# Optimization experiments

Hardware: AMD Instinct MI355X
Metric: run time of the kernel (lower is better)

## Reference

```python
import jax, jax.numpy as jnp
import numpy as np

CTX_LEN = 7
TAU = 2.0      # curr_temp = max_temp at init
ALPHA = -1.0   # dist_to_logits_alpha


def _prelu(v, a):
    return jnp.where(v >= 0, v, a * v)


def setup_inputs() -> dict:
    key = jax.random.key(0)
    ks = jax.random.split(key, 8)
    B, T, D, M = 8, 4096, 256, 1024
    x = jax.random.normal(ks[0], (B, T, D), dtype=jnp.float32)
    noise = jax.random.normal(ks[1], (B, D, T - 1 + CTX_LEN), dtype=jnp.float32)
    gumbel_u = jax.random.uniform(ks[2], (B * T, M), dtype=jnp.float32)
    embedding = jax.random.uniform(ks[3], (1, M, D), dtype=jnp.float32)  # nn.init.uniform_
    w_ctx = jax.random.normal(ks[4], (D, D, CTX_LEN), dtype=jnp.float32) * 0.02
    w_f1 = jax.random.normal(ks[5], (D, 2 * D), dtype=jnp.float32) * 0.04
    w_f2 = jax.random.normal(ks[6], (D, 2 * D), dtype=jnp.float32) * 0.04
    a1 = jnp.array(0.5, dtype=jnp.float32)
    a2 = jnp.array(0.5, dtype=jnp.float32)
    return {"x": x, "noise": noise, "gumbel_u": gumbel_u, "epo": 10,
            "embedding": embedding, "w_ctx": w_ctx, "w_f1": w_f1, "a1": a1,
            "w_f2": w_f2, "a2": a2}


def reference(x, noise, gumbel_u, epo, embedding, w_ctx, w_f1, a1, w_f2, a2):
    B, T, D = x.shape
    E = embedding[0]                      # [M, D]
    M = E.shape[0]
    xt = jnp.transpose(x, (0, 2, 1))      # [B, D, T]
    # context input: x[:, :-1] permuted, left-padded by 1+7-1=7, detached
    ctx_in = jax.lax.stop_gradient(jnp.pad(xt[:, :, :T - 1], ((0, 0), (0, 0), (CTX_LEN, 0))))
    scale = jnp.sqrt(jnp.mean(ctx_in ** 2, axis=(1, 2), keepdims=True))
    ctx_in_noisy = jax.lax.stop_gradient(ctx_in + 0.5 * scale * noise * (0.5 ** (epo / 10.0)))
    ctx_out = jax.lax.conv_general_dilated(
        ctx_in_noisy, w_ctx, (1,), 'VALID',
        dimension_numbers=('NCH', 'OIH', 'NCH'))   # [B, D, T]
    # fuse 1 (1x1 conv == channel matmul) + PReLU
    cat1 = jnp.concatenate([xt, ctx_out], axis=1)            # [B, 2D, T]
    cur = _prelu(jnp.einsum('oc,bct->bot', w_f1, cat1), a1)  # [B, D, T]
    cur = jnp.transpose(cur, (0, 2, 1)).reshape(-1, D)       # [B*T, D]
    # squared distances via addmm equivalent, scaled to logits
    dist = (jnp.sum(cur ** 2, axis=1, keepdims=True)
            + jnp.sum(E ** 2, axis=1)
            - 2.0 * cur @ E.T)                               # [B*T, M]
    dm = ALPHA * dist
    # hard code usage entropy
    k = jnp.argmax(dm, axis=-1)
    hard_probs = jnp.mean(jax.nn.one_hot(k, M, dtype=dm.dtype), axis=0)
    code_perplexity = -jnp.sum(hard_probs * jnp.log2(hard_probs + 1e-10))
    # soft usage entropy
    avg_probs = jnp.mean(jax.nn.softmax(dm, axis=-1), axis=0)
    prob_perplexity = -jnp.sum(avg_probs * jnp.log2(avg_probs + 1e-10))
    # hard gumbel-softmax (straight-through)
    u = jnp.clip(gumbel_u, 1e-10, 1.0 - 1e-7)
    g = -jnp.log(-jnp.log(u))
    y_soft = jax.nn.softmax((dm + g) / TAU, axis=-1)
    idx = jnp.argmax(y_soft, axis=-1)
    y_hard = jax.nn.one_hot(idx, M, dtype=y_soft.dtype)
    dm_st = y_hard - jax.lax.stop_gradient(y_soft) + y_soft  # [B*T, M]
    quantization_inds = idx.reshape(B, T, 1)
    # dequantize: one-hot (straight-through) times codebook
    out_q = (dm_st @ E).reshape(B, T, D)
    # fuse 2 + PReLU
    cat2 = jnp.concatenate([jnp.transpose(out_q, (0, 2, 1)), ctx_out], axis=1)
    quantized = jnp.transpose(_prelu(jnp.einsum('oc,bct->bot', w_f2, cat2), a2), (0, 2, 1))
    return quantized, code_perplexity, prob_perplexity, quantization_inds
```

## Files before the change

kernel.cpp:

```cpp
#include <hip/hip_runtime.h>
#include <cmath>

#define B_    8
#define T_    4096
#define D_    256
#define M_    1024
#define L_    4102
#define LP_   4104
#define CTX_  7
#define NROW_ 32768

constexpr size_t OFF_DM    = 0;
constexpr size_t OFF_XT    = 0;
constexpr size_t OFF_CTXN  = 33554432;
constexpr size_t OFF_CURT  = 33554432;
constexpr size_t OFF_CTXO  = OFF_CTXN + (size_t)B_ * D_ * LP_;
constexpr size_t OFF_CUR2  = OFF_CTXO + (size_t)B_ * D_ * T_;
constexpr size_t OFF_SOFT  = OFF_CUR2 + NROW_;
constexpr size_t OFF_HIST  = OFF_SOFT + 4096;
constexpr size_t OFF_SUMSQ = OFF_HIST + 1024;
constexpr size_t OFF_ESQ   = OFF_SUMSQ + 16;
constexpr size_t OFF_IDX   = OFF_ESQ + 1024;
constexpr size_t OFF_ET    = OFF_IDX + NROW_;
constexpr size_t OFF_W1T   = OFF_ET + 262144;
constexpr size_t OFF_W2T   = OFF_W1T + 131072;
constexpr size_t OFF_WCT   = OFF_W2T + 131072;
constexpr size_t OFF_P     = OFF_WCT + 458752;

using s16x8 = __attribute__((ext_vector_type(8))) short;
using f32x4 = __attribute__((ext_vector_type(4))) float;

__device__ __forceinline__ ushort bf16rne(float f) {
  uint u = __float_as_uint(f);
  u += 0x7fffu + ((u >> 16) & 1u);
  return (ushort)(u >> 16);
}
__device__ __forceinline__ float bf16tof(ushort h) {
  return __uint_as_float((uint)h << 16);
}

__global__ __launch_bounds__(256) void k_prep(const float* __restrict__ emb,
                                              const float* __restrict__ wf1,
                                              const float* __restrict__ wf2,
                                              const float* __restrict__ wctx,
                                              const float* __restrict__ x,
                                              float* __restrict__ ET,
                                              float* __restrict__ W1T,
                                              float* __restrict__ W2T,
                                              ushort* __restrict__ WPF,
                                              float* __restrict__ esq,
                                              float* __restrict__ sumsq) {
  const int id = blockIdx.x;
  if (id < 512) {
    __shared__ float tile[32][33];
    const int tx = threadIdx.x & 31, ty = threadIdx.x >> 5;
    const float* src; float* dst; int R, C, c0, r0;
    if (id < 256)      { src = emb;  dst = ET;  R = 1024; C = 256;  c0 = (id & 7) << 5;  r0 = (id >> 3) << 5; }
    else if (id < 384) { const int r = id - 256; src = wf1; dst = W1T; R = 256; C = 512; c0 = (r & 15) << 5; r0 = (r >> 4) << 5; }
    else               { const int r = id - 384; src = wf2; dst = W2T; R = 256; C = 512; c0 = (r & 15) << 5; r0 = (r >> 4) << 5; }
    for (int rr = ty; rr < 32; rr += 8) {
      const int rI = r0 + rr, cI = c0 + tx;
      tile[rr][tx] = (rI < R && cI < C) ? src[(size_t)rI * C + cI] : 0.f;
    }
    __syncthreads();
    for (int rr = ty; rr < 32; rr += 8) {
      const int cI = c0 + rr, rI = r0 + tx;
      if (cI < C && rI < R) dst[(size_t)cI * R + rI] = tile[tx][rr];
    }
  } else if (id < 736) {
    const int K8 = id - 512;
    const int h = K8 >> 5, j = K8 & 31;
    const int o = threadIdx.x;
    uint hp[4], lp[4];
    #pragma unroll
    for (int e2 = 0; e2 < 4; ++e2) {
      ushort hs[2], ls[2];
      #pragma unroll
      for (int k = 0; k < 2; ++k) {
        const int i = (j << 3) + (e2 << 1) + k;
        const float v = wctx[(size_t)o * 1792 + (size_t)i * 7 + h];
        const ushort hb = bf16rne(v);
        hs[k] = hb;
        ls[k] = bf16rne(v - bf16tof(hb));
      }
      hp[e2] = (uint)hs[0] | ((uint)hs[1] << 16);
      lp[e2] = (uint)ls[0] | ((uint)ls[1] << 16);
    }
    uint4* W = (uint4*)WPF;
    W[(size_t)(K8 * 2) * 256 + o]     = make_uint4(hp[0], hp[1], hp[2], hp[3]);
    W[(size_t)(K8 * 2 + 1) * 256 + o] = make_uint4(lp[0], lp[1], lp[2], lp[3]);
  } else if (id < 992) {
    const int row = ((id - 736) << 2) + (threadIdx.x >> 6);
    const int lane = threadIdx.x & 63;
    const float4 v = ((const float4*)emb)[((size_t)row << 6) + lane];
    float s = v.x * v.x + v.y * v.y + v.z * v.z + v.w * v.w;
    #pragma unroll
    for (int off = 32; off; off >>= 1) s += __shfl_down(s, off, 64);
    if (lane == 0) esq[row] = s;
  } else {
    const int chunk = id - 992;
    const int b = chunk >> 6, sub = chunk & 63;
    const float4* xb = (const float4*)(x + (size_t)b * T_ * D_);
    const int N4 = (T_ - 1) * D_ / 4;
    float s = 0.f;
    for (int j = sub * 256 + threadIdx.x; j < N4; j += 64 * 256) {
      float4 v = xb[j];
      s += v.x * v.x + v.y * v.y + v.z * v.z + v.w * v.w;
    }
    #pragma unroll
    for (int off = 32; off; off >>= 1) s += __shfl_down(s, off, 64);
    __shared__ float red[4];
    const int lane = threadIdx.x & 63, wv = threadIdx.x >> 6;
    if (lane == 0) red[wv] = s;
    __syncthreads();
    if (threadIdx.x == 0) atomicAdd(&sumsq[b], (red[0] + red[1]) + (red[2] + red[3]));
  }
}

__global__ __launch_bounds__(256) void k_noisy(const float* __restrict__ x,
                                               const float* __restrict__ noise,
                                               const int* __restrict__ epo,
                                               const float* __restrict__ sumsq,
                                               ushort* __restrict__ inT,
                                               float* __restrict__ xT) {
  const int b = blockIdx.z;
  const int i0 = blockIdx.y << 5;
  const int tau0 = blockIdx.x << 5;
  const int tx = threadIdx.x & 31, ty = threadIdx.x >> 5;
  __shared__ float xt[32][33];
  __shared__ float nz[32][33];
  const int tr0 = tau0 - CTX_;
  for (int r = ty; r < 32; r += 8) {
    const int t = tr0 + r;
    xt[r][tx] = (t >= 0 && t < T_) ? x[((size_t)b * T_ + t) * D_ + i0 + tx] : 0.f;
  }
  for (int r = ty; r < 32; r += 8) {
    const int tau = tau0 + tx;
    nz[r][tx] = (tau < L_) ? noise[((size_t)b * D_ + i0 + r) * L_ + tau] : 0.f;
  }
  __syncthreads();
  const float scale = sqrtf(sumsq[b] * (1.0f / (256.0f * 4102.0f)));
  const float coef = 0.5f * powf(0.5f, (float)epo[0] * 0.1f) * scale;
  for (int r = ty; r < 32; r += 8) {
    const int i = i0 + r;
    const int tau = tau0 + tx;
    const float xv = xt[tx][r];
    if (tau >= CTX_ && tau < T_ + CTX_)
      xT[((size_t)b * D_ + i) * T_ + (tau - CTX_)] = xv;
  }
  if (threadIdx.x < 128) {
    const int tau_r = threadIdx.x >> 2, jl = threadIdx.x & 3;
    const int tau = tau0 + tau_r;
    if (tau < L_) {
      uint hp[4], lp[4];
      #pragma unroll
      for (int e2 = 0; e2 < 4; ++e2) {
        ushort hs[2], ls[2];
        #pragma unroll
        for (int k = 0; k < 2; ++k) {
          const int ir = (jl << 3) + (e2 << 1) + k;
          const float v = coef * nz[ir][tau_r] + xt[tau_r][ir];
          const ushort hb = bf16rne(v);
          hs[k] = hb;
          ls[k] = bf16rne(v - bf16tof(hb));
        }
        hp[e2] = (uint)hs[0] | ((uint)hs[1] << 16);
        lp[e2] = (uint)ls[0] | ((uint)ls[1] << 16);
      }
      const int j = (i0 >> 3) + jl;
      const int jsw = j ^ (tau & 7);
      ushort* dst = inT + ((size_t)b * LP_ + tau) * 256 + (jsw << 3);
      *(uint4*)dst = make_uint4(hp[0], hp[1], hp[2], hp[3]);
      *(uint4*)(dst + (size_t)B_ * LP_ * 256) = make_uint4(lp[0], lp[1], lp[2], lp[3]);
    }
  }
}

__global__ __launch_bounds__(256, 2) void k_convm(const ushort* __restrict__ WPF,
                                                  const ushort* __restrict__ inT,
                                                  float* __restrict__ ctxo) {
  const int t0 = blockIdx.x << 6;
  const int b  = blockIdx.y;
  const int tid = threadIdx.x;
  const int lane = tid & 63;
  const int wv = tid >> 6;
  const int ln = lane & 15, lg = lane >> 4;
  __shared__ ushort sB[2 * 72 * 256];
  {
    const size_t rb = ((size_t)b * LP_ + t0) * 256;
    const uint4* s4h = (const uint4*)(inT + rb);
    const uint4* s4l = (const uint4*)(inT + (size_t)B_ * LP_ * 256 + rb);
    uint4* d4 = (uint4*)sB;
    for (int q = tid; q < 2304; q += 256) d4[q] = s4h[q];
    for (int q = tid; q < 2304; q += 256) d4[2304 + q] = s4l[q];
  }
  __syncthreads();

  const f32x4 fz = {0.f, 0.f, 0.f, 0.f};
  f32x4 acc[4][4];
  #pragma unroll
  for (int i = 0; i < 4; ++i)
    #pragma unroll
    for (int j = 0; j < 4; ++j) acc[i][j] = fz;

  const ushort* wp = WPF + ((size_t)lg * 512 + (wv << 6) + ln) * 8;

  #pragma unroll 1
  for (int h = 0; h < 7; ++h) {
    #pragma unroll 1
    for (int js = 0; js < 8; ++js) {
      const int K8b = (h << 5) + (js << 2);
      s16x8 Af[2][4];
      #pragma unroll
      for (int to = 0; to < 4; ++to) {
        const ushort* ap = wp + (size_t)(K8b * 512 + (to << 4)) * 8;
        Af[0][to] = *(const s16x8*)ap;
        Af[1][to] = *(const s16x8*)(ap + 2048);
      }
      s16x8 Bf[2][4];
      #pragma unroll
      for (int tt = 0; tt < 4; ++tt) {
        const int r = (tt << 4) + ln + h;
        const int jsw = ((js << 2) + lg) ^ (r & 7);
        const int e0 = r * 256 + (jsw << 3);
        Bf[0][tt] = *(const s16x8*)&sB[e0];
        Bf[1][tt] = *(const s16x8*)&sB[18432 + e0];
      }
      #pragma unroll
      for (int to = 0; to < 4; ++to)
        #pragma unroll
        for (int tt = 0; tt < 4; ++tt) {
          acc[to][tt] = __builtin_amdgcn_mfma_f32_16x16x32_bf16(Af[0][to], Bf[0][tt], acc[to][tt], 0, 0, 0);
          acc[to][tt] = __builtin_amdgcn_mfma_f32_16x16x32_bf16(Af[0][to], Bf[1][tt], acc[to][tt], 0, 0, 0);
          acc[to][tt] = __builtin_amdgcn_mfma_f32_16x16x32_bf16(Af[1][to], Bf[0][tt], acc[to][tt], 0, 0, 0);
        }
    }
  }
  float* cb = ctxo + ((size_t)b * 256 + (wv << 6)) * T_ + t0;
  #pragma unroll
  for (int to = 0; to < 4; ++to)
    #pragma unroll
    for (int tt = 0; tt < 4; ++tt)
      #pragma unroll
      for (int rg = 0; rg < 4; ++rg) {
        const int o_loc = (to << 4) + (lg << 2) + rg;
        cb[(size_t)o_loc * T_ + (tt << 4) + ln] = acc[to][tt][rg];
      }
}

__device__ __forceinline__ void stage16x128(float* __restrict__ dst,
                                            const float* __restrict__ src,
                                            const int gstride, const int tid) {
  #pragma unroll
  for (int p = 0; p < 2; ++p) {
    const int q = p * 256 + tid;
    const int r = q >> 5, c = (q & 31) << 2;
    *(float4*)&dst[(r << 7) + c] = *(const float4*)&src[(size_t)r * gstride + c];
  }
}

__device__ __forceinline__ void gemm16s(const float* __restrict__ sA,
                                        const float* __restrict__ sB,
                                        const int ay, const int bx4,
                                        float acc[8][8]) {
  #pragma unroll 4
  for (int c = 0; c < 16; ++c) {
    const float4 a0 = *(const float4*)&sA[(c << 7) + ay];
    const float4 a1 = *(const float4*)&sA[(c << 7) + ay + 4];
    const float4 b0 = *(const float4*)&sB[(c << 7) + bx4];
    const float4 b1 = *(const float4*)&sB[(c << 7) + bx4 + 64];
    const float av[8] = {a0.x, a0.y, a0.z, a0.w, a1.x, a1.y, a1.z, a1.w};
    const float bv[8] = {b0.x, b0.y, b0.z, b0.w, b1.x, b1.y, b1.z, b1.w};
    #pragma unroll
    for (int i = 0; i < 8; ++i)
      #pragma unroll
      for (int j = 0; j < 8; ++j)
        acc[i][j] = fmaf(av[i], bv[j], acc[i][j]);
  }
}

__global__ __launch_bounds__(256) void k_fuse1(const float* __restrict__ xT,
                                               const float* __restrict__ ctxo,
                                               const float* __restrict__ w1T,
                                               const float* __restrict__ a1,
                                               float* __restrict__ curT,
                                               float* __restrict__ cur2) {
  const int bk = blockIdx.x;
  const int b = bk >> 5;
  const int t0 = (bk & 31) << 7;
  const int o0 = blockIdx.y << 7;
  const int tid = threadIdx.x;
  const int tx = tid & 15, ty = tid >> 4;
  const int ox = ty << 3, tp4 = tx << 2;
  __shared__ float smem[4096];
  float* sW = smem;
  float* sX = smem + 2048;
  float acc[8][8] = {};
  for (int cc = 0; cc < 512; cc += 16) {
    __syncthreads();
    stage16x128(sW, w1T + (size_t)cc * 256 + o0, 256, tid);
    const float* xsrc = (cc < 256)
        ? xT + ((size_t)b * D_ + cc) * T_ + t0
        : ctxo + ((size_t)b * D_ + (cc - 256)) * T_ + t0;
    stage16x128(sX, xsrc, T_, tid);
    __syncthreads();
    gemm16s(sW, sX, ox, tp4, acc);
  }
  const float alpha = a1[0];
  const size_t row0 = (size_t)b * T_ + t0;
  float part[8] = {};
  #pragma unroll
  for (int oo = 0; oo < 8; ++oo) {
    #pragma unroll
    for (int j = 0; j < 8; ++j) {
      float v = acc[oo][j];
      v = (v >= 0.f) ? v : alpha * v;
      acc[oo][j] = v;
      part[j] = fmaf(v, v, part[j]);
    }
    const float4 v0 = {acc[oo][0], acc[oo][1], acc[oo][2], acc[oo][3]};
    const float4 v1 = {acc[oo][4], acc[oo][5], acc[oo][6], acc[oo][7]};
    float* dst = curT + (size_t)(o0 + ox + oo) * NROW_ + row0;
    *(float4*)(dst + tp4) = v0;
    *(float4*)(dst + tp4 + 64) = v1;
  }
  __syncthreads();
  float* red = smem;
  #pragma unroll
  for (int j = 0; j < 4; ++j) {
    red[(tp4 + j) * 17 + ty] = part[j];
    red[(tp4 + 64 + j) * 17 + ty] = part[4 + j];
  }
  __syncthreads();
  if (tid < 128) {
    float s = 0.f;
    #pragma unroll
    for (int k = 0; k < 16; ++k) s += red[tid * 17 + k];
    atomicAdd(&cur2[row0 + tid], s);
  }
}

__global__ __launch_bounds__(256) void k_pmm(const float* __restrict__ ET,
                                             const float* __restrict__ w2T,
                                             float* __restrict__ P) {
  const int m0 = blockIdx.x << 7;
  const int o0 = blockIdx.y << 7;
  const int tid = threadIdx.x;
  const int tx = tid & 15, ty = tid >> 4;
  const int my = ty << 3, ox4 = tx << 2;
  __shared__ float smem[4096];
  float* sM = smem;
  float* sW = smem + 2048;
  float acc[8][8] = {};
  for (int cc = 0; cc < 256; cc += 16) {
    __syncthreads();
    stage16x128(sM, ET + (size_t)cc * M_ + m0, M_, tid);
    stage16x128(sW, w2T + (size_t)cc * 256 + o0, 256, tid);
    __syncthreads();
    gemm16s(sM, sW, my, ox4, acc);
  }
  #pragma unroll
  for (int mm = 0; mm < 8; ++mm) {
    const float4 v0 = {acc[mm][0], acc[mm][1], acc[mm][2], acc[mm][3]};
    const float4 v1 = {acc[mm][4], acc[mm][5], acc[mm][6], acc[mm][7]};
    float* dst = P + (size_t)(m0 + my + mm) * 256 + o0;
    *(float4*)(dst + ox4) = v0;
    *(float4*)(dst + ox4 + 64) = v1;
  }
}

__global__ __launch_bounds__(256) void k_dist(const float* __restrict__ curT,
                                              const float* __restrict__ ET,
                                              const float* __restrict__ cur2,
                                              const float* __restrict__ esq,
                                              float* __restrict__ dm) {
  const int r0 = blockIdx.x << 7;
  const int m0 = blockIdx.y << 7;
  const int tid = threadIdx.x;
  const int tx = tid & 15, ty = tid >> 4;
  const int ry = ty << 3, mx4 = tx << 2;
  __shared__ float smem[4096];
  float* sC = smem;
  float* sE = smem + 2048;
  float acc[8][8] = {};
  for (int cc = 0; cc < 256; cc += 16) {
    __syncthreads();
    stage16x128(sC, curT + (size_t)cc * NROW_ + r0, NROW_, tid);
    stage16x128(sE, ET + (size_t)cc * M_ + m0, M_, tid);
    __syncthreads();
    gemm16s(sC, sE, ry, mx4, acc);
  }
  float c2[8], eq0[4], eq1[4];
  *(float4*)&c2[0] = *(const float4*)&cur2[r0 + ry];
  *(float4*)&c2[4] = *(const float4*)&cur2[r0 + ry + 4];
  *(float4*)&eq0[0] = *(const float4*)&esq[m0 + mx4];
  *(float4*)&eq1[0] = *(const float4*)&esq[m0 + mx4 + 64];
  #pragma unroll
  for (int rr = 0; rr < 8; ++rr) {
    float o0v[4], o1v[4];
    #pragma unroll
    for (int j = 0; j < 4; ++j) {
      o0v[j] = -(c2[rr] + eq0[j] - 2.0f * acc[rr][j]);
      o1v[j] = -(c2[rr] + eq1[j] - 2.0f * acc[rr][j + 4]);
    }
    float* dst = dm + (size_t)(r0 + ry + rr) * M_ + m0;
    *(float4*)(dst + mx4) = *(float4*)&o0v[0];
    *(float4*)(dst + mx4 + 64) = *(float4*)&o1v[0];
  }
}

__global__ __launch_bounds__(256) void k_soft(const float* __restrict__ dm,
                                              const float* __restrict__ gu,
                                              float* __restrict__ soft4,
                                              unsigned* __restrict__ hist,
                                              int* __restrict__ idxi,
                                              float* __restrict__ idxf) {
  const int tid = threadIdx.x;
  const int lane = tid & 63, w = tid >> 6;
  __shared__ float accS[1024];
  __shared__ unsigned histS[1024];
  for (int j = tid; j < 1024; j += 256) { accS[j] = 0.f; histS[j] = 0u; }
  __syncthreads();
  float p[16] = {};
  const int rbase = (blockIdx.x << 6) + (w << 4);
  for (int rr = 0; rr < 16; ++rr) {
    const int r = rbase + rr;
    const float4* dr = (const float4*)(dm + ((size_t)r << 10));
    float v[16];
    #pragma unroll
    for (int k = 0; k < 4; ++k) {
      const float4 d = dr[lane + (k << 6)];
      v[k * 4 + 0] = d.x; v[k * 4 + 1] = d.y; v[k * 4 + 2] = d.z; v[k * 4 + 3] = d.w;
    }
    float mx = v[0];
    #pragma unroll
    for (int s = 1; s < 16; ++s) mx = fmaxf(mx, v[s]);
    #pragma unroll
    for (int m = 32; m; m >>= 1) mx = fmaxf(mx, __shfl_xor(mx, m, 64));
    float e[16]; float sum = 0.f;
    #pragma unroll
    for (int s = 0; s < 16; ++s) { e[s] = expf(v[s] - mx); sum += e[s]; }
    #pragma unroll
    for (int m = 32; m; m >>= 1) sum += __shfl_xor(sum, m, 64);
    const float inv = 1.0f / sum;
    #pragma unroll
    for (int s = 0; s < 16; ++s) p[s] = fmaf(e[s], inv, p[s]);
    float bv = v[0]; int bi = (lane << 2);
    #pragma unroll
    for (int s = 1; s < 16; ++s) {
      const int m_ = (lane << 2) + ((s >> 2) << 8) + (s & 3);
      if (v[s] > bv) { bv = v[s]; bi = m_; }
    }
    #pragma unroll
    for (int m = 32; m; m >>= 1) {
      const float ov = __shfl_xor(bv, m, 64);
      const int oi = __shfl_xor(bi, m, 64);
      if (ov > bv || (ov == bv && oi < bi)) { bv = ov; bi = oi; }
    }
    if (lane == 0) atomicAdd(&histS[bi], 1u);
    const float4* gr = (const float4*)(gu + ((size_t)r << 10));
    float z[16];
    #pragma unroll
    for (int k = 0; k < 4; ++k) {
      const float4 u = gr[lane + (k << 6)];
      const float uu[4] = {u.x, u.y, u.z, u.w};
      #pragma unroll
      for (int j = 0; j < 4; ++j) {
        const float uc = fminf(fmaxf(uu[j], 1e-10f), 1.0f - 1e-7f);
        z[k * 4 + j] = v[k * 4 + j] - logf(-logf(uc));
      }
    }
    bv = z[0]; bi = (lane << 2);
    #pragma unroll
    for (int s = 1; s < 16; ++s) {
      const int m_ = (lane << 2) + ((s >> 2) << 8) + (s & 3);
      if (z[s] > bv) { bv = z[s]; bi = m_; }
    }
    #pragma unroll
    for (int m = 32; m; m >>= 1) {
      const float ov = __shfl_xor(bv, m, 64);
      const int oi = __shfl_xor(bi, m, 64);
      if (ov > bv || (ov == bv && oi < bi)) { bv = ov; bi = oi; }
    }
    if (lane == 0) { idxi[r] = bi; idxf[r] = (float)bi; }
  }
  #pragma unroll
  for (int s = 0; s < 16; ++s)
    atomicAdd(&accS[(lane << 2) + ((s >> 2) << 8) + (s & 3)], p[s]);
  __syncthreads();
  const int rep = (blockIdx.x & 3) << 10;
  for (int j = tid; j < 1024; j += 256) {
    atomicAdd(&soft4[rep + j], accS[j]);
    const unsigned h = histS[j];
    if (h) atomicAdd(&hist[j], h);
  }
}

__global__ __launch_bounds__(256) void k_perp(const float* __restrict__ soft4,
                                              const unsigned* __restrict__ hist,
                                              float* __restrict__ out2) {
  const int tid = threadIdx.x;
  float cp = 0.f, pp = 0.f;
  for (int m = tid; m < 1024; m += 256) {
    const float hp = (float)hist[m] * (1.0f / 32768.0f);
    cp += hp * log2f(hp + 1e-10f);
    const float q = (soft4[m] + soft4[1024 + m] + soft4[2048 + m] + soft4[3072 + m]) * (1.0f / 32768.0f);
    pp += q * log2f(q + 1e-10f);
  }
  #pragma unroll
  for (int off = 32; off; off >>= 1) {
    cp += __shfl_down(cp, off, 64);
    pp += __shfl_down(pp, off, 64);
  }
  __shared__ float rc[4], rp[4];
  const int lane = tid & 63, wv = tid >> 6;
  if (lane == 0) { rc[wv] = cp; rp[wv] = pp; }
  __syncthreads();
  if (tid == 0) {
    out2[0] = -((rc[0] + rc[1]) + (rc[2] + rc[3]));
    out2[1] = -((rp[0] + rp[1]) + (rp[2] + rp[3]));
  }
}

__global__ __launch_bounds__(256) void k_fuse2(const float* __restrict__ ctxo,
                                               const float* __restrict__ w2T,
                                               const float* __restrict__ P,
                                               const int* __restrict__ idxi,
                                               const float* __restrict__ a2,
                                               float* __restrict__ outq) {
  const int bk = blockIdx.x;
  const int b = bk >> 5;
  const int t0 = (bk & 31) << 7;
  const int o0 = blockIdx.y << 7;
  const int tid = threadIdx.x;
  const int tx = tid & 15, ty = tid >> 4;
  const int ay = ty << 3, ox4 = tx << 2;
  __shared__ float smem[4096];
  __shared__ int idxS[128];
  float* sX = smem;
  float* sW = smem + 2048;
  if (tid < 128) idxS[tid] = idxi[(size_t)b * T_ + t0 + tid];
  float acc[8][8] = {};
  for (int cc = 0; cc < 256; cc += 16) {
    __syncthreads();
    stage16x128(sX, ctxo + ((size_t)b * D_ + cc) * T_ + t0, T_, tid);
    stage16x128(sW, w2T + (size_t)(256 + cc) * 256 + o0, 256, tid);
    __syncthreads();
    gemm16s(sX, sW, ay, ox4, acc);
  }
  const float alpha = a2[0];
  #pragma unroll
  for (int tt = 0; tt < 8; ++tt) {
    const int id = idxS[ay + tt];
    const float* pr = P + (size_t)id * 256 + o0;
    const float4 p0 = *(const float4*)(pr + ox4);
    const float4 p1 = *(const float4*)(pr + ox4 + 64);
    const float pv[8] = {p0.x, p0.y, p0.z, p0.w, p1.x, p1.y, p1.z, p1.w};
    float o[8];
    #pragma unroll
    for (int oo = 0; oo < 8; ++oo) {
      const float v = acc[tt][oo] + pv[oo];
      o[oo] = (v >= 0.f) ? v : alpha * v;
    }
    float* dst = outq + ((size_t)b * T_ + t0 + ay + tt) * D_ + o0;
    *(float4*)(dst + ox4) = *(float4*)&o[0];
    *(float4*)(dst + ox4 + 64) = *(float4*)&o[4];
  }
}

extern "C" void kernel_launch(void* const* d_in, const int* in_sizes, int n_in,
                              void* d_out, int out_size, void* d_ws, size_t ws_size,
                              hipStream_t stream) {
  (void)in_sizes; (void)n_in; (void)out_size; (void)ws_size;
  const float* x     = (const float*)d_in[0];
  const float* noise = (const float*)d_in[1];
  const float* gu    = (const float*)d_in[2];
  const int*   epo   = (const int*)d_in[3];
  const float* emb   = (const float*)d_in[4];
  const float* wctx  = (const float*)d_in[5];
  const float* wf1   = (const float*)d_in[6];
  const float* a1    = (const float*)d_in[7];
  const float* wf2   = (const float*)d_in[8];
  const float* a2    = (const float*)d_in[9];

  float* ws    = (float*)d_ws;
  float* dm    = ws + OFF_DM;
  float* xT    = ws + OFF_XT;
  ushort* inT  = (ushort*)(ws + OFF_CTXN);
  float* curT  = ws + OFF_CURT;
  float* ctxo  = ws + OFF_CTXO;
  float* cur2  = ws + OFF_CUR2;
  float* soft  = ws + OFF_SOFT;
  unsigned* hist = (unsigned*)(ws + OFF_HIST);
  float* sumsq = ws + OFF_SUMSQ;
  float* esq   = ws + OFF_ESQ;
  int*   idxi  = (int*)(ws + OFF_IDX);
  float* ET    = ws + OFF_ET;
  float* W1T   = ws + OFF_W1T;
  float* W2T   = ws + OFF_W2T;
  ushort* WPF  = (ushort*)(ws + OFF_WCT);
  float* P     = ws + OFF_P;

  float* outq = (float*)d_out;
  float* scal = outq + (size_t)NROW_ * D_;
  float* idxf = scal + 2;

  hipMemsetAsync(ws + OFF_CUR2, 0, (NROW_ + 4096 + 1024 + 16) * sizeof(float), stream);

  k_prep  <<<1504, 256, 0, stream>>>(emb, wf1, wf2, wctx, x, ET, W1T, W2T, WPF, esq, sumsq);
  k_noisy <<<dim3(129, 8, 8), 256, 0, stream>>>(x, noise, epo, sumsq, inT, xT);
  k_convm <<<dim3(64, 8), 256, 0, stream>>>(WPF, inT, ctxo);
  k_fuse1 <<<dim3(256, 2), 256, 0, stream>>>(xT, ctxo, W1T, a1, curT, cur2);
  k_pmm   <<<dim3(8, 2), 256, 0, stream>>>(ET, W2T, P);
  k_dist  <<<dim3(256, 8), 256, 0, stream>>>(curT, ET, cur2, esq, dm);
  k_soft  <<<512, 256, 0, stream>>>(dm, gu, soft, hist, idxi, idxf);
  k_perp  <<<1, 256, 0, stream>>>(soft, hist, scal);
  k_fuse2 <<<dim3(256, 2), 256, 0, stream>>>(ctxo, W2T, P, idxi, a2, outq);
}
```

Baseline: 813.7 us.

## Rewrite fuse2 GEMM with bf16 MFMA and direct global fragment loads

Replaces the fp32 shared-memory tiled GEMM in the second fuse stage with bf16 MFMA 16x16x32 instructions. Operands are loaded straight from global memory and rounded to bf16 per lane, with no LDS staging. Each block now covers 64 timesteps across all 256 output channels, spread over four wavefronts. This trades fp32 precision for matrix-core throughput, and the strided, uncoalesced global loads and repeated conversions may limit the gain.

```diff
diff --git a/kernel.cpp b/kernel.cpp
--- a/kernel.cpp
+++ b/kernel.cpp
@@ -522,49 +522,74 @@
   }
 }
 
-__global__ __launch_bounds__(256) void k_fuse2(const float* __restrict__ ctxo,
-                                               const float* __restrict__ w2T,
-                                               const float* __restrict__ P,
-                                               const int* __restrict__ idxi,
-                                               const float* __restrict__ a2,
-                                               float* __restrict__ outq) {
+__global__ __launch_bounds__(256) void k_fuse2m(const float* __restrict__ ctxo,
+                                                const float* __restrict__ w2T,
+                                                const float* __restrict__ P,
+                                                const int* __restrict__ idxi,
+                                                const float* __restrict__ a2,
+                                                float* __restrict__ outq) {
   const int bk = blockIdx.x;
-  const int b = bk >> 5;
-  const int t0 = (bk & 31) << 7;
-  const int o0 = blockIdx.y << 7;
+  const int b = bk >> 6;
+  const int t0 = (bk & 63) << 6;
   const int tid = threadIdx.x;
-  const int tx = tid & 15, ty = tid >> 4;
-  const int ay = ty << 3, ox4 = tx << 2;
-  __shared__ float smem[4096];
-  __shared__ int idxS[128];
-  float* sX = smem;
-  float* sW = smem + 2048;
-  if (tid < 128) idxS[tid] = idxi[(size_t)b * T_ + t0 + tid];
-  float acc[8][8] = {};
-  for (int cc = 0; cc < 256; cc += 16) {
-    __syncthreads();
-    stage16x128(sX, ctxo + ((size_t)b * D_ + cc) * T_ + t0, T_, tid);
-    stage16x128(sW, w2T + (size_t)(256 + cc) * 256 + o0, 256, tid);
-    __syncthreads();
-    gemm16s(sX, sW, ay, ox4, acc);
-  }
+  const int lane = tid & 63, wv = tid >> 6;
+  const int ln = lane & 15, lg = lane >> 4;
+  const int o0w = wv << 6;
+  __shared__ int idxS[64];
+  if (tid < 64) idxS[tid] = idxi[(size_t)b * T_ + t0 + tid];
+  __syncthreads();
+
+  const f32x4 fz = {0.f, 0.f, 0.f, 0.f};
+  f32x4 acc[4][4];
+  #pragma unroll
+  for (int i = 0; i < 4; ++i)
+    #pragma unroll
+    for (int j = 0; j < 4; ++j) acc[i][j] = fz;
+
+  #pragma unroll 1
+  for (int ks = 0; ks < 8; ++ks) {
+    const int cb = (ks << 5) + (lg << 3);
+    s16x8 Af[4];
+    #pragma unroll
+    for (int to = 0; to < 4; ++to) {
+      const float* wp = w2T + (size_t)(256 + cb) * 256 + o0w + (to << 4) + ln;
+      #pragma unroll
+      for (int e = 0; e < 8; ++e)
+        Af[to][e] = (short)bf16rne(wp[(size_t)e * 256]);
+    }
+    s16x8 Bf[4];
+    #pragma unroll
+    for (int tt = 0; tt < 4; ++tt) {
+      const float* xp = ctxo + ((size_t)b * D_ + cb) * T_ + t0 + (tt << 4) + ln;
+      #pragma unroll
+      for (int e = 0; e < 8; ++e)
+        Bf[tt][e] = (short)bf16rne(xp[(size_t)e * T_]);
+    }
+    #pragma unroll
+    for (int to = 0; to < 4; ++to)
+      #pragma unroll
+      for (int tt = 0; tt < 4; ++tt)
+        acc[to][tt] = __builtin_amdgcn_mfma_f32_16x16x32_bf16(Af[to], Bf[tt], acc[to][tt], 0, 0, 0);
+  }
+
   const float alpha = a2[0];
   #pragma unroll
-  for (int tt = 0; tt < 8; ++tt) {
-    const int id = idxS[ay + tt];
-    const float* pr = P + (size_t)id * 256 + o0;
-    const float4 p0 = *(const float4*)(pr + ox4);
-    const float4 p1 = *(const float4*)(pr + ox4 + 64);
-    const float pv[8] = {p0.x, p0.y, p0.z, p0.w, p1.x, p1.y, p1.z, p1.w};
-    float o[8];
-    #pragma unroll
-    for (int oo = 0; oo < 8; ++oo) {
-      const float v = acc[tt][oo] + pv[oo];
-      o[oo] = (v >= 0.f) ? v : alpha * v;
-    }
-    float* dst = outq + ((size_t)b * T_ + t0 + ay + tt) * D_ + o0;
-    *(float4*)(dst + ox4) = *(float4*)&o[0];
-    *(float4*)(dst + ox4 + 64) = *(float4*)&o[4];
+  for (int tt = 0; tt < 4; ++tt) {
+    const int t = t0 + (tt << 4) + ln;
+    const int id = idxS[(tt << 4) + ln];
+    #pragma unroll
+    for (int to = 0; to < 4; ++to) {
+      const int ob = o0w + (to << 4) + (lg << 2);
+      const float4 p4 = *(const float4*)&P[(size_t)id * 256 + ob];
+      const float pv[4] = {p4.x, p4.y, p4.z, p4.w};
+      float o[4];
+      #pragma unroll
+      for (int rg = 0; rg < 4; ++rg) {
+        const float v = acc[to][tt][rg] + pv[rg];
+        o[rg] = (v >= 0.f) ? v : alpha * v;
+      }
+      *(float4*)&outq[((size_t)b * T_ + t) * D_ + ob] = *(float4*)&o[0];
+    }
   }
 }
 
@@ -615,5 +640,5 @@
   k_dist  <<<dim3(256, 8), 256, 0, stream>>>(curT, ET, cur2, esq, dm);
   k_soft  <<<512, 256, 0, stream>>>(dm, gu, soft, hist, idxi, idxf);
   k_perp  <<<1, 256, 0, stream>>>(soft, hist, scal);
-  k_fuse2 <<<dim3(256, 2), 256, 0, stream>>>(ctxo, W2T, P, idxi, a2, outq);
-}
+  k_fuse2m<<<512, 256, 0, stream>>>(ctxo, W2T, P, idxi, a2, outq);
+}
```

Result: faster. 790.0 us (-2.9%).
